# Kernel tuning notes

Measured on AMD Instinct MI355X. Metric: run time of the kernel, lower is better.

## Reference

```python
import jax, jax.numpy as jnp
import numpy as np

N_NODES = 50000
N_EDGES = 800000
IN_CH, HID_CH, OUT_CH = 128, 128, 64


def setup_inputs() -> dict:
    key = jax.random.key(0)
    k1, k2, k3, k4, k5, k6 = jax.random.split(key, 6)
    x = jax.random.normal(k1, (N_NODES, IN_CH), dtype=jnp.float32)
    edge_index = jax.random.randint(k2, (2, N_EDGES), 0, N_NODES, dtype=jnp.int64)
    # nn.Linear params: W [out, in], b [out]
    W1 = jax.random.normal(k3, (HID_CH, IN_CH), dtype=jnp.float32) / np.sqrt(IN_CH)
    b1 = jax.random.normal(k4, (HID_CH,), dtype=jnp.float32) * 0.01
    W2 = jax.random.normal(k5, (OUT_CH, HID_CH), dtype=jnp.float32) / np.sqrt(HID_CH)
    b2 = jax.random.normal(k6, (OUT_CH,), dtype=jnp.float32) * 0.01
    return {"x": x, "edge_index": edge_index, "W1": W1, "b1": b1, "W2": W2, "b2": b2}


def _aggregate(x, edge_index):
    # Faithful to SimpleGNN.aggregate: deg from ROW counts, normalization gathered at DST (col).
    row, col = edge_index[0], edge_index[1]
    n = x.shape[0]
    deg = jnp.bincount(row, length=n).astype(x.dtype)
    deg_inv = jnp.where(deg > 0, 1.0 / deg, 0.0)
    # out[dst] += x[src] * deg_inv[dst]  ==  segment_sum(x[src] by dst) * deg_inv[dst]
    agg = jax.ops.segment_sum(x[row], col, num_segments=n)
    return agg * deg_inv[:, None]


def reference(x, edge_index, W1, b1, W2, b2):
    h = x @ W1.T + b1                 # [N, hidden]
    h = _aggregate(h, edge_index)     # degree-normalized scatter-add
    out = h @ W2.T + b2               # [N, out]
    return out
```

## Files before the change

kernel.cpp:

```cpp
#include <hip/hip_runtime.h>
#include <hip/hip_bf16.h>


#define IN_CH   128
#define OUT_CH  64
#define NCHUNK  128
#define LGCHUNK 7
#define NRANGE  4
#define RBINS   12544
#define MC_BLOCKS 33

typedef unsigned short u16;
typedef unsigned int u32;

static __device__ inline float bfu32_lo(u32 u) {
    u32 v = u << 16; return __uint_as_float(v);
}
static __device__ inline float bfu32_hi(u32 u) {
    u32 v = u & 0xffff0000u; return __uint_as_float(v);
}
static __device__ inline u16 f2bf(float f) {
    __hip_bfloat16 h = __float2bfloat16(f);
    return *reinterpret_cast<u16*>(&h);
}

static __device__ inline int detect_stride(const int* ei) {
    int f = 1;
    for (int i = 1; i < 64; i += 2)
        if (ei[i] != 0) { f = 0; break; }
    return 1 + f;
}

__global__ __launch_bounds__(256) void mk_prep(const float* __restrict__ W1,
                                               const float* __restrict__ b1,
                                               const float* __restrict__ W2,
                                               const int* __restrict__ ei,
                                               float* __restrict__ M,
                                               float* __restrict__ c,
                                               u16* __restrict__ row_slab,
                                               u16* __restrict__ col_slab,
                                               int n_edges, int n_nodes) {
    __shared__ u32 bins[RBINS];
    __shared__ int s_stride;
    int b = blockIdx.x;
    if (b < MC_BLOCKS) {
        int tid = b * 256 + threadIdx.x;
        if (tid < IN_CH * OUT_CH) {
            int o = tid & (OUT_CH - 1);
            int i = tid >> 6;
            float acc = 0.f;
            for (int h = 0; h < 128; ++h)
                acc += W1[h * 128 + i] * W2[o * 128 + h];
            M[i * OUT_CH + o] = acc;
        } else if (tid < IN_CH * OUT_CH + OUT_CH) {
            int o = tid - IN_CH * OUT_CH;
            float acc = 0.f;
            for (int h = 0; h < 128; ++h)
                acc += b1[h] * W2[o * 128 + h];
            c[o] = acc;
        }
        return;
    }
    int hb = b - MC_BLOCKS;
    int chunk = hb & (NCHUNK - 1);
    int range = hb >> LGCHUNK;

    int range_size = (n_nodes + NRANGE - 1) / NRANGE;
    int lo = range * range_size;
    int hi = lo + range_size; if (hi > n_nodes) hi = n_nodes;
    int nbins = hi - lo;
    if (nbins <= 0) return;

    if (threadIdx.x == 0) s_stride = detect_stride(ei);
    for (int i = threadIdx.x; i < nbins; i += 256) bins[i] = 0u;
    __syncthreads();
    int stride = s_stride;

    size_t e0 = (size_t)chunk * n_edges / NCHUNK;
    size_t e1 = (size_t)(chunk + 1) * n_edges / NCHUNK;
    size_t cnt = e1 - e0;
    const int* rp = ei;
    const int* cp = ei + (size_t)n_edges * stride;

    size_t i = threadIdx.x;
    int s[8], d[8];
    for (; i + 1792 < cnt; i += 2048) {
#pragma unroll
        for (int k = 0; k < 8; ++k) s[k] = rp[(e0 + i + 256 * k) * stride];
#pragma unroll
        for (int k = 0; k < 8; ++k) d[k] = cp[(e0 + i + 256 * k) * stride];
#pragma unroll
        for (int k = 0; k < 8; ++k) {
            if (s[k] >= lo && s[k] < hi) atomicAdd(&bins[s[k] - lo], 1u);
            if (d[k] >= lo && d[k] < hi && (unsigned)s[k] < (unsigned)n_nodes)
                atomicAdd(&bins[d[k] - lo], 0x10000u);
        }
    }
    for (; i < cnt; i += 256) {
        int ss = rp[(e0 + i) * stride];
        int dd = cp[(e0 + i) * stride];
        if (ss >= lo && ss < hi) atomicAdd(&bins[ss - lo], 1u);
        if (dd >= lo && dd < hi && (unsigned)ss < (unsigned)n_nodes)
            atomicAdd(&bins[dd - lo], 0x10000u);
    }
    __syncthreads();

    size_t base = (size_t)chunk * n_nodes + lo;
    for (int k = threadIdx.x; k < nbins; k += 256) {
        u32 v = bins[k];
        row_slab[base + k] = (u16)(v & 0xFFFFu);
        col_slab[base + k] = (u16)(v >> 16);
    }
}

__global__ __launch_bounds__(256) void mk_y_choff(const float* __restrict__ x,
                                                  const float* __restrict__ M,
                                                  u16* __restrict__ y,
                                                  u16* __restrict__ row_slab,
                                                  u16* __restrict__ col_slab,
                                                  int* __restrict__ deg_row,
                                                  int* __restrict__ cnt_col,
                                                  int* __restrict__ cursor_part,
                                                  int* __restrict__ bsums,
                                                  int n_nodes, int y_blocks) {
    __shared__ float smem[IN_CH * OUT_CH + 64 * (IN_CH + 4)];
    int b = blockIdx.x;
    int tid = threadIdx.x;

    if (b < y_blocks) {
        float* Ms = smem;
        float (*xs)[IN_CH + 4] = (float(*)[IN_CH + 4])(smem + IN_CH * OUT_CH);
        int tx = tid & 15;
        int ty = tid >> 4;
        int row0 = b * 64;

        const float4* Mv = (const float4*)M;
        float4* Msv = (float4*)Ms;
#pragma unroll
        for (int k = 0; k < 8; ++k) Msv[tid + 256 * k] = Mv[tid + 256 * k];

        for (int f = tid; f < 64 * 32; f += 256) {
            int r = f >> 5, kq = f & 31;
            float4 v = make_float4(0.f, 0.f, 0.f, 0.f);
            if (row0 + r < n_nodes)
                v = *(const float4*)&x[(size_t)(row0 + r) * IN_CH + 4 * kq];
            *(float4*)&xs[r][4 * kq] = v;
        }
        __syncthreads();

        float4 acc[4];
#pragma unroll
        for (int j = 0; j < 4; ++j) acc[j] = make_float4(0.f, 0.f, 0.f, 0.f);

        for (int k = 0; k < IN_CH; k += 4) {
            float4 xr[4], mr[4];
#pragma unroll
            for (int j = 0; j < 4; ++j)
                xr[j] = *(const float4*)&xs[4 * ty + j][k];
#pragma unroll
            for (int kk = 0; kk < 4; ++kk)
                mr[kk] = *(const float4*)&Ms[(k + kk) * OUT_CH + 4 * tx];
#pragma unroll
            for (int j = 0; j < 4; ++j) {
                acc[j].x = fmaf(xr[j].x, mr[0].x, acc[j].x);
                acc[j].y = fmaf(xr[j].x, mr[0].y, acc[j].y);
                acc[j].z = fmaf(xr[j].x, mr[0].z, acc[j].z);
                acc[j].w = fmaf(xr[j].x, mr[0].w, acc[j].w);
                acc[j].x = fmaf(xr[j].y, mr[1].x, acc[j].x);
                acc[j].y = fmaf(xr[j].y, mr[1].y, acc[j].y);
                acc[j].z = fmaf(xr[j].y, mr[1].z, acc[j].z);
                acc[j].w = fmaf(xr[j].y, mr[1].w, acc[j].w);
                acc[j].x = fmaf(xr[j].z, mr[2].x, acc[j].x);
                acc[j].y = fmaf(xr[j].z, mr[2].y, acc[j].y);
                acc[j].z = fmaf(xr[j].z, mr[2].z, acc[j].z);
                acc[j].w = fmaf(xr[j].z, mr[2].w, acc[j].w);
                acc[j].x = fmaf(xr[j].w, mr[3].x, acc[j].x);
                acc[j].y = fmaf(xr[j].w, mr[3].y, acc[j].y);
                acc[j].z = fmaf(xr[j].w, mr[3].z, acc[j].z);
                acc[j].w = fmaf(xr[j].w, mr[3].w, acc[j].w);
            }
        }

#pragma unroll
        for (int j = 0; j < 4; ++j) {
            int r = row0 + 4 * ty + j;
            if (r < n_nodes) {
                ushort4 s4;
                s4.x = f2bf(acc[j].x);
                s4.y = f2bf(acc[j].y);
                s4.z = f2bf(acc[j].z);
                s4.w = f2bf(acc[j].w);
                *(ushort4*)&y[(size_t)r * OUT_CH + 4 * tx] = s4;
            }
        }
        return;
    }

    int* sm = (int*)smem;
    int t = tid;
    int n = (b - y_blocks) * 256 + t;
    int run = 0;
    if (n < n_nodes) {
        int sum = 0;
#pragma unroll 8
        for (int ch = 0; ch < NCHUNK; ++ch)
            sum += row_slab[(size_t)ch * n_nodes + n];
        deg_row[n] = sum;
#pragma unroll 8
        for (int ch = 0; ch < NCHUNK; ++ch) {
            int v = col_slab[(size_t)ch * n_nodes + n];
            col_slab[(size_t)ch * n_nodes + n] = (u16)run;
            run += v;
        }
        cnt_col[n] = run;
    }
    sm[t] = run;
    __syncthreads();
    for (int d = 1; d < 256; d <<= 1) {
        int add = (t >= d) ? sm[t - d] : 0;
        __syncthreads();
        sm[t] += add;
        __syncthreads();
    }
    if (n < n_nodes) cursor_part[n] = sm[t] - run;
    if (t == 255) bsums[b - y_blocks] = sm[t];
}

static __device__ inline void block_bscan(const int* __restrict__ bsums, int nb,
                                          int* __restrict__ bscan) {
    int t = threadIdx.x;
    int v = (t < nb) ? bsums[t] : 0;
    bscan[t] = v;
    __syncthreads();
    for (int d = 1; d < 256; d <<= 1) {
        int add = (t >= d) ? bscan[t - d] : 0;
        __syncthreads();
        bscan[t] += add;
        __syncthreads();
    }
    bscan[t] -= v;
    __syncthreads();
}

__global__ __launch_bounds__(256) void mk_place(const int* __restrict__ ei,
                                                const int* __restrict__ cursor_part,
                                                const int* __restrict__ bsums,
                                                const u16* __restrict__ col_slab,
                                                int* __restrict__ csr_src,
                                                int n_edges, int n_nodes, int nb) {
    __shared__ int rank[RBINS];
    __shared__ int bscan[256];
    block_bscan(bsums, nb, bscan);

    int b = blockIdx.x;
    int chunk = b & (NCHUNK - 1);
    int range = b >> LGCHUNK;

    int range_size = (n_nodes + NRANGE - 1) / NRANGE;
    int lo = range * range_size;
    int hi = lo + range_size; if (hi > n_nodes) hi = n_nodes;
    if (hi <= lo) return;

    for (int i = threadIdx.x; i < hi - lo; i += 256) rank[i] = 0;
    __syncthreads();

    int stride = detect_stride(ei);
    size_t e0 = (size_t)chunk * n_edges / NCHUNK;
    size_t e1 = (size_t)(chunk + 1) * n_edges / NCHUNK;
    size_t cnt = e1 - e0;
    const int* rp = ei;
    const int* cp = ei + (size_t)n_edges * stride;
    size_t slab_base = (size_t)chunk * n_nodes;

    size_t i = threadIdx.x;
    int s[8], d[8], cpart[8], coff[8];
    for (; i + 1792 < cnt; i += 2048) {
#pragma unroll
        for (int k = 0; k < 8; ++k) s[k] = rp[(e0 + i + 256 * k) * stride];
#pragma unroll
        for (int k = 0; k < 8; ++k) d[k] = cp[(e0 + i + 256 * k) * stride];
#pragma unroll
        for (int k = 0; k < 8; ++k) {
            int dc = (d[k] >= lo && d[k] < hi) ? d[k] : lo;
            cpart[k] = cursor_part[dc];
            coff[k]  = (int)col_slab[slab_base + dc];
        }
#pragma unroll
        for (int k = 0; k < 8; ++k) {
            if (d[k] >= lo && d[k] < hi && (unsigned)s[k] < (unsigned)n_nodes) {
                int r = atomicAdd(&rank[d[k] - lo], 1);
                csr_src[cpart[k] + bscan[d[k] >> 8] + coff[k] + r] = s[k];
            }
        }
    }
    for (; i < cnt; i += 256) {
        int ss = rp[(e0 + i) * stride];
        int dd = cp[(e0 + i) * stride];
        if (dd >= lo && dd < hi && (unsigned)ss < (unsigned)n_nodes) {
            int r = atomicAdd(&rank[dd - lo], 1);
            csr_src[cursor_part[dd] + bscan[dd >> 8] + (int)col_slab[slab_base + dd] + r] = ss;
        }
    }
}

__global__ __launch_bounds__(256) void mk_agg_final(const int* __restrict__ cursor_part,
                                                    const int* __restrict__ bsums,
                                                    const int* __restrict__ cnt_col,
                                                    const int* __restrict__ csr_src,
                                                    const int* __restrict__ deg_row,
                                                    const uint2* __restrict__ yv,
                                                    const float* __restrict__ c,
                                                    const float* __restrict__ b2,
                                                    float* __restrict__ out,
                                                    int n_nodes, int nb) {
    __shared__ int bscan[256];
    block_bscan(bsums, nb, bscan);

    int wave = threadIdx.x >> 6;
    int lane = threadIdx.x & 63;
    int dsub = lane >> 4;
    int ch   = lane & 15;
    int d = blockIdx.x * 16 + wave * 4 + dsub;
    if (d >= n_nodes) return;

    int start = cursor_part[d] + bscan[d >> 8];
    int cnt = cnt_col[d];
    int end = start + cnt;
    int e1m = end - 1;
    float a0 = 0.f, a1 = 0.f, a2 = 0.f, a3 = 0.f;
    for (int j = start; j < end; j += 8) {
        int idx[8], srcs[8];
#pragma unroll
        for (int k = 0; k < 8; ++k) {
            int t = j + k;
            idx[k] = t > e1m ? e1m : t;
        }
#pragma unroll
        for (int k = 0; k < 8; ++k) srcs[k] = csr_src[idx[k]];
        uint2 u[8];
#pragma unroll
        for (int k = 0; k < 8; ++k) u[k] = yv[(size_t)srcs[k] * 16 + ch];
#pragma unroll
        for (int k = 1; k < 8; ++k)
            if (j + k >= end) { u[k].x = 0u; u[k].y = 0u; }
#pragma unroll
        for (int k = 0; k < 8; ++k) {
            a0 += bfu32_lo(u[k].x);
            a1 += bfu32_hi(u[k].x);
            a2 += bfu32_lo(u[k].y);
            a3 += bfu32_hi(u[k].y);
        }
    }
    int dr = deg_row[d];
    float di = (dr > 0) ? (1.0f / (float)dr) : 0.f;
    float fc = di * (float)cnt;
    float4 cv = ((const float4*)c)[ch];
    float4 bv = ((const float4*)b2)[ch];
    float4 o;
    o.x = di * a0 + fc * cv.x + bv.x;
    o.y = di * a1 + fc * cv.y + bv.y;
    o.z = di * a2 + fc * cv.z + bv.z;
    o.w = di * a3 + fc * cv.w + bv.w;
    ((float4*)(out + (size_t)d * OUT_CH))[ch] = o;
}

extern "C" void kernel_launch(void* const* d_in, const int* in_sizes, int n_in,
                              void* d_out, int out_size, void* d_ws, size_t ws_size,
                              hipStream_t stream) {
    const float* x  = (const float*)d_in[0];
    const int*   ei = (const int*)d_in[1];
    const float* W1 = (const float*)d_in[2];
    const float* b1 = (const float*)d_in[3];
    const float* W2 = (const float*)d_in[4];
    const float* b2 = (const float*)d_in[5];
    float* out = (float*)d_out;

    const int n_nodes = in_sizes[0] / IN_CH;
    const int n_edges = in_sizes[1] / 2;

    const size_t slab_bytes = (((size_t)NCHUNK * n_nodes * 2) + 127) & ~(size_t)127;
    const size_t csr_bytes  = ((size_t)n_edges * 4 + 127) & ~(size_t)127;

    char* ws = (char*)d_ws;
    float* M        = (float*)(ws);
    float* c        = (float*)(ws + 32768);
    int*   deg_row  = (int*)  (ws + 33152);
    int*   cnt_col  = (int*)  (ws + 233216);
    int*   cursor   = (int*)  (ws + 433280);
    int*   bsums    = (int*)  (ws + 633344);
    u16*   row_slab = (u16*)  (ws + 637440);
    u16*   col_slab = (u16*)  (ws + 637440 + slab_bytes);
    int*   csr_src  = (int*)  (ws + 637440 + 2 * slab_bytes);
    u16*   y        = (u16*)  (ws + 637440 + 2 * slab_bytes + csr_bytes);

    const int y_blocks = (n_nodes + 63) / 64;
    const int nb = (n_nodes + 255) / 256;

    mk_prep<<<MC_BLOCKS + NCHUNK * NRANGE, 256, 0, stream>>>(
        W1, b1, W2, ei, M, c, row_slab, col_slab, n_edges, n_nodes);

    mk_y_choff<<<y_blocks + nb, 256, 0, stream>>>(
        x, M, y, row_slab, col_slab, deg_row, cnt_col, cursor, bsums,
        n_nodes, y_blocks);

    mk_place<<<NCHUNK * NRANGE, 256, 0, stream>>>(
        ei, cursor, bsums, col_slab, csr_src, n_edges, n_nodes, nb);

    mk_agg_final<<<(n_nodes + 15) / 16, 256, 0, stream>>>(
        cursor, bsums, cnt_col, csr_src, deg_row, (const uint2*)y, c, b2, out,
        n_nodes, nb);
}
```

Baseline: 163.7 us.

## Fuse four pipeline kernels into one cooperative persistent kernel with grid syncs

Replaces the four separate launches (prep/histogram, y-GEMM plus count offsets, CSR placement, aggregation) with one cooperative kernel of 512 blocks. The stages are separated by grid-wide barriers, and blocks loop over the work items of each stage. NCHUNK drops from 128 to 112 so the histogram and placement stages fit inside the persistent grid, and stride detection now uses a wave ballot. The aim is to remove kernel launch gaps and tail effects between stages. In exchange, grid syncs cost time, and the persistent grid of 2 blocks per CU with large LDS may limit latency hiding in the gather-heavy aggregation. If the cooperative launch fails, the code falls back to the old four-kernel path.

New measurement: 371.8 us. 2.27x slower.

```diff
diff --git a/kernel.cpp b/kernel.cpp
--- a/kernel.cpp
+++ b/kernel.cpp
@@ -1,80 +1,74 @@
 #include <hip/hip_runtime.h>
 #include <hip/hip_bf16.h>
+#include <hip/hip_cooperative_groups.h>
+
+namespace cg = cooperative_groups;
 
 
 #define IN_CH   128
 #define OUT_CH  64
-#define NCHUNK  128
-#define LGCHUNK 7
+#define NCHUNK  112
 #define NRANGE  4
 #define RBINS   12544
 #define MC_BLOCKS 33
+#define GRID    512
+#define SMEM_FLOATS (IN_CH * OUT_CH + 64 * (IN_CH + 4))
 
 typedef unsigned short u16;
 typedef unsigned int u32;
 
-static __device__ inline float bfu32_lo(u32 u) {
-    u32 v = u << 16; return __uint_as_float(v);
-}
-static __device__ inline float bfu32_hi(u32 u) {
-    u32 v = u & 0xffff0000u; return __uint_as_float(v);
-}
+static __device__ inline float bfu32_lo(u32 u) { return __uint_as_float(u << 16); }
+static __device__ inline float bfu32_hi(u32 u) { return __uint_as_float(u & 0xffff0000u); }
 static __device__ inline u16 f2bf(float f) {
     __hip_bfloat16 h = __float2bfloat16(f);
     return *reinterpret_cast<u16*>(&h);
 }
 
-static __device__ inline int detect_stride(const int* ei) {
-    int f = 1;
-    for (int i = 1; i < 64; i += 2)
-        if (ei[i] != 0) { f = 0; break; }
-    return 1 + f;
-}
-
-__global__ __launch_bounds__(256) void mk_prep(const float* __restrict__ W1,
-                                               const float* __restrict__ b1,
-                                               const float* __restrict__ W2,
-                                               const int* __restrict__ ei,
-                                               float* __restrict__ M,
-                                               float* __restrict__ c,
-                                               u16* __restrict__ row_slab,
-                                               u16* __restrict__ col_slab,
-                                               int n_edges, int n_nodes) {
-    __shared__ u32 bins[RBINS];
-    __shared__ int s_stride;
-    int b = blockIdx.x;
-    if (b < MC_BLOCKS) {
-        int tid = b * 256 + threadIdx.x;
-        if (tid < IN_CH * OUT_CH) {
-            int o = tid & (OUT_CH - 1);
-            int i = tid >> 6;
-            float acc = 0.f;
-            for (int h = 0; h < 128; ++h)
-                acc += W1[h * 128 + i] * W2[o * 128 + h];
-            M[i * OUT_CH + o] = acc;
-        } else if (tid < IN_CH * OUT_CH + OUT_CH) {
-            int o = tid - IN_CH * OUT_CH;
-            float acc = 0.f;
-            for (int h = 0; h < 128; ++h)
-                acc += b1[h] * W2[o * 128 + h];
-            c[o] = acc;
-        }
-        return;
-    }
-    int hb = b - MC_BLOCKS;
-    int chunk = hb & (NCHUNK - 1);
-    int range = hb >> LGCHUNK;
-
+static __device__ inline int detect_stride_wave(const int* __restrict__ ei) {
+    int lane = threadIdx.x & 63;
+    int idx = (lane < 32) ? (2 * lane + 1) : 1;
+    int v = ei[idx];
+    unsigned long long m = __ballot((v != 0) && (lane < 32));
+    return (m == 0ull) ? 2 : 1;
+}
+
+static __device__ void ph_Mc(int b, int tid,
+                             const float* __restrict__ W1, const float* __restrict__ b1,
+                             const float* __restrict__ W2,
+                             float* __restrict__ M, float* __restrict__ c) {
+    int t = b * 256 + tid;
+    if (t < IN_CH * OUT_CH) {
+        int o = t & (OUT_CH - 1);
+        int i = t >> 6;
+        float acc = 0.f;
+        for (int h = 0; h < 128; ++h)
+            acc += W1[h * 128 + i] * W2[o * 128 + h];
+        M[i * OUT_CH + o] = acc;
+    } else if (t < IN_CH * OUT_CH + OUT_CH) {
+        int o = t - IN_CH * OUT_CH;
+        float acc = 0.f;
+        for (int h = 0; h < 128; ++h)
+            acc += b1[h] * W2[o * 128 + h];
+        c[o] = acc;
+    }
+}
+
+static __device__ void ph_hist(int j, int tid, float* __restrict__ smem,
+                               const int* __restrict__ ei,
+                               u16* __restrict__ row_slab, u16* __restrict__ col_slab,
+                               int n_edges, int n_nodes) {
+    u32* bins = (u32*)smem;
+    int chunk = j % NCHUNK;
+    int range = j / NCHUNK;
     int range_size = (n_nodes + NRANGE - 1) / NRANGE;
     int lo = range * range_size;
     int hi = lo + range_size; if (hi > n_nodes) hi = n_nodes;
     int nbins = hi - lo;
     if (nbins <= 0) return;
 
-    if (threadIdx.x == 0) s_stride = detect_stride(ei);
-    for (int i = threadIdx.x; i < nbins; i += 256) bins[i] = 0u;
-    __syncthreads();
-    int stride = s_stride;
+    int stride = detect_stride_wave(ei);
+    for (int i = tid; i < nbins; i += 256) bins[i] = 0u;
+    __syncthreads();
 
     size_t e0 = (size_t)chunk * n_edges / NCHUNK;
     size_t e1 = (size_t)(chunk + 1) * n_edges / NCHUNK;
@@ -82,7 +76,7 @@
     const int* rp = ei;
     const int* cp = ei + (size_t)n_edges * stride;
 
-    size_t i = threadIdx.x;
+    size_t i = tid;
     int s[8], d[8];
     for (; i + 1792 < cnt; i += 2048) {
 #pragma unroll
@@ -106,99 +100,92 @@
     __syncthreads();
 
     size_t base = (size_t)chunk * n_nodes + lo;
-    for (int k = threadIdx.x; k < nbins; k += 256) {
+    for (int k = tid; k < nbins; k += 256) {
         u32 v = bins[k];
         row_slab[base + k] = (u16)(v & 0xFFFFu);
         col_slab[base + k] = (u16)(v >> 16);
     }
 }
 
-__global__ __launch_bounds__(256) void mk_y_choff(const float* __restrict__ x,
-                                                  const float* __restrict__ M,
-                                                  u16* __restrict__ y,
-                                                  u16* __restrict__ row_slab,
-                                                  u16* __restrict__ col_slab,
-                                                  int* __restrict__ deg_row,
-                                                  int* __restrict__ cnt_col,
-                                                  int* __restrict__ cursor_part,
-                                                  int* __restrict__ bsums,
-                                                  int n_nodes, int y_blocks) {
-    __shared__ float smem[IN_CH * OUT_CH + 64 * (IN_CH + 4)];
-    int b = blockIdx.x;
-    int tid = threadIdx.x;
-
-    if (b < y_blocks) {
-        float* Ms = smem;
-        float (*xs)[IN_CH + 4] = (float(*)[IN_CH + 4])(smem + IN_CH * OUT_CH);
-        int tx = tid & 15;
-        int ty = tid >> 4;
-        int row0 = b * 64;
-
-        const float4* Mv = (const float4*)M;
-        float4* Msv = (float4*)Ms;
-#pragma unroll
-        for (int k = 0; k < 8; ++k) Msv[tid + 256 * k] = Mv[tid + 256 * k];
-
-        for (int f = tid; f < 64 * 32; f += 256) {
-            int r = f >> 5, kq = f & 31;
-            float4 v = make_float4(0.f, 0.f, 0.f, 0.f);
-            if (row0 + r < n_nodes)
-                v = *(const float4*)&x[(size_t)(row0 + r) * IN_CH + 4 * kq];
-            *(float4*)&xs[r][4 * kq] = v;
-        }
-        __syncthreads();
-
-        float4 acc[4];
-#pragma unroll
-        for (int j = 0; j < 4; ++j) acc[j] = make_float4(0.f, 0.f, 0.f, 0.f);
-
-        for (int k = 0; k < IN_CH; k += 4) {
-            float4 xr[4], mr[4];
-#pragma unroll
-            for (int j = 0; j < 4; ++j)
-                xr[j] = *(const float4*)&xs[4 * ty + j][k];
-#pragma unroll
-            for (int kk = 0; kk < 4; ++kk)
-                mr[kk] = *(const float4*)&Ms[(k + kk) * OUT_CH + 4 * tx];
-#pragma unroll
-            for (int j = 0; j < 4; ++j) {
-                acc[j].x = fmaf(xr[j].x, mr[0].x, acc[j].x);
-                acc[j].y = fmaf(xr[j].x, mr[0].y, acc[j].y);
-                acc[j].z = fmaf(xr[j].x, mr[0].z, acc[j].z);
-                acc[j].w = fmaf(xr[j].x, mr[0].w, acc[j].w);
-                acc[j].x = fmaf(xr[j].y, mr[1].x, acc[j].x);
-                acc[j].y = fmaf(xr[j].y, mr[1].y, acc[j].y);
-                acc[j].z = fmaf(xr[j].y, mr[1].z, acc[j].z);
-                acc[j].w = fmaf(xr[j].y, mr[1].w, acc[j].w);
-                acc[j].x = fmaf(xr[j].z, mr[2].x, acc[j].x);
-                acc[j].y = fmaf(xr[j].z, mr[2].y, acc[j].y);
-                acc[j].z = fmaf(xr[j].z, mr[2].z, acc[j].z);
-                acc[j].w = fmaf(xr[j].z, mr[2].w, acc[j].w);
-                acc[j].x = fmaf(xr[j].w, mr[3].x, acc[j].x);
-                acc[j].y = fmaf(xr[j].w, mr[3].y, acc[j].y);
-                acc[j].z = fmaf(xr[j].w, mr[3].z, acc[j].z);
-                acc[j].w = fmaf(xr[j].w, mr[3].w, acc[j].w);
-            }
-        }
-
+static __device__ void ph_ytile(int t, int tid, float* __restrict__ smem,
+                                const float* __restrict__ x, const float* __restrict__ M,
+                                u16* __restrict__ y, int n_nodes) {
+    __syncthreads();
+    float* Ms = smem;
+    float (*xs)[IN_CH + 4] = (float(*)[IN_CH + 4])(smem + IN_CH * OUT_CH);
+    int tx = tid & 15;
+    int ty = tid >> 4;
+    int row0 = t * 64;
+
+    const float4* Mv = (const float4*)M;
+    float4* Msv = (float4*)Ms;
+#pragma unroll
+    for (int k = 0; k < 8; ++k) Msv[tid + 256 * k] = Mv[tid + 256 * k];
+
+    for (int f = tid; f < 64 * 32; f += 256) {
+        int r = f >> 5, kq = f & 31;
+        float4 v = make_float4(0.f, 0.f, 0.f, 0.f);
+        if (row0 + r < n_nodes)
+            v = *(const float4*)&x[(size_t)(row0 + r) * IN_CH + 4 * kq];
+        *(float4*)&xs[r][4 * kq] = v;
+    }
+    __syncthreads();
+
+    float4 acc[4];
+#pragma unroll
+    for (int j = 0; j < 4; ++j) acc[j] = make_float4(0.f, 0.f, 0.f, 0.f);
+
+    for (int k = 0; k < IN_CH; k += 4) {
+        float4 xr[4], mr[4];
+#pragma unroll
+        for (int j = 0; j < 4; ++j)
+            xr[j] = *(const float4*)&xs[4 * ty + j][k];
+#pragma unroll
+        for (int kk = 0; kk < 4; ++kk)
+            mr[kk] = *(const float4*)&Ms[(k + kk) * OUT_CH + 4 * tx];
 #pragma unroll
         for (int j = 0; j < 4; ++j) {
-            int r = row0 + 4 * ty + j;
-            if (r < n_nodes) {
-                ushort4 s4;
-                s4.x = f2bf(acc[j].x);
-                s4.y = f2bf(acc[j].y);
-                s4.z = f2bf(acc[j].z);
-                s4.w = f2bf(acc[j].w);
-                *(ushort4*)&y[(size_t)r * OUT_CH + 4 * tx] = s4;
-            }
-        }
-        return;
-    }
-
+            acc[j].x = fmaf(xr[j].x, mr[0].x, acc[j].x);
+            acc[j].y = fmaf(xr[j].x, mr[0].y, acc[j].y);
+            acc[j].z = fmaf(xr[j].x, mr[0].z, acc[j].z);
+            acc[j].w = fmaf(xr[j].x, mr[0].w, acc[j].w);
+            acc[j].x = fmaf(xr[j].y, mr[1].x, acc[j].x);
+            acc[j].y = fmaf(xr[j].y, mr[1].y, acc[j].y);
+            acc[j].z = fmaf(xr[j].y, mr[1].z, acc[j].z);
+            acc[j].w = fmaf(xr[j].y, mr[1].w, acc[j].w);
+            acc[j].x = fmaf(xr[j].z, mr[2].x, acc[j].x);
+            acc[j].y = fmaf(xr[j].z, mr[2].y, acc[j].y);
+            acc[j].z = fmaf(xr[j].z, mr[2].z, acc[j].z);
+            acc[j].w = fmaf(xr[j].z, mr[2].w, acc[j].w);
+            acc[j].x = fmaf(xr[j].w, mr[3].x, acc[j].x);
+            acc[j].y = fmaf(xr[j].w, mr[3].y, acc[j].y);
+            acc[j].z = fmaf(xr[j].w, mr[3].z, acc[j].z);
+            acc[j].w = fmaf(xr[j].w, mr[3].w, acc[j].w);
+        }
+    }
+
+#pragma unroll
+    for (int j = 0; j < 4; ++j) {
+        int r = row0 + 4 * ty + j;
+        if (r < n_nodes) {
+            ushort4 s4;
+            s4.x = f2bf(acc[j].x);
+            s4.y = f2bf(acc[j].y);
+            s4.z = f2bf(acc[j].z);
+            s4.w = f2bf(acc[j].w);
+            *(ushort4*)&y[(size_t)r * OUT_CH + 4 * tx] = s4;
+        }
+    }
+}
+
+static __device__ void ph_choff(int jj, int tid, float* __restrict__ smem,
+                                u16* __restrict__ row_slab, u16* __restrict__ col_slab,
+                                int* __restrict__ deg_row, int* __restrict__ cnt_col,
+                                int* __restrict__ cursor_part, int* __restrict__ bsums,
+                                int n_nodes) {
+    __syncthreads();
     int* sm = (int*)smem;
-    int t = tid;
-    int n = (b - y_blocks) * 256 + t;
+    int n = jj * 256 + tid;
     int run = 0;
     if (n < n_nodes) {
         int sum = 0;
@@ -214,20 +201,20 @@
         }
         cnt_col[n] = run;
     }
-    sm[t] = run;
+    sm[tid] = run;
     __syncthreads();
     for (int d = 1; d < 256; d <<= 1) {
-        int add = (t >= d) ? sm[t - d] : 0;
+        int add = (tid >= d) ? sm[tid - d] : 0;
         __syncthreads();
-        sm[t] += add;
+        sm[tid] += add;
         __syncthreads();
     }
-    if (n < n_nodes) cursor_part[n] = sm[t] - run;
-    if (t == 255) bsums[b - y_blocks] = sm[t];
-}
-
-static __device__ inline void block_bscan(const int* __restrict__ bsums, int nb,
-                                          int* __restrict__ bscan) {
+    if (n < n_nodes) cursor_part[n] = sm[tid] - run;
+    if (tid == 255) bsums[jj] = sm[tid];
+}
+
+static __device__ void block_bscan(const int* __restrict__ bsums, int nb,
+                                   int* __restrict__ bscan) {
     int t = threadIdx.x;
     int v = (t < nb) ? bsums[t] : 0;
     bscan[t] = v;
@@ -242,29 +229,28 @@
     __syncthreads();
 }
 
-__global__ __launch_bounds__(256) void mk_place(const int* __restrict__ ei,
-                                                const int* __restrict__ cursor_part,
-                                                const int* __restrict__ bsums,
-                                                const u16* __restrict__ col_slab,
-                                                int* __restrict__ csr_src,
-                                                int n_edges, int n_nodes, int nb) {
-    __shared__ int rank[RBINS];
-    __shared__ int bscan[256];
+static __device__ void ph_place(int j, int tid, float* __restrict__ smem,
+                                const int* __restrict__ ei,
+                                const int* __restrict__ cursor_part,
+                                const int* __restrict__ bsums,
+                                const u16* __restrict__ col_slab,
+                                int* __restrict__ csr_src,
+                                int n_edges, int n_nodes, int nb) {
+    int* rank = (int*)smem;
+    int* bscan = (int*)smem + RBINS;
     block_bscan(bsums, nb, bscan);
 
-    int b = blockIdx.x;
-    int chunk = b & (NCHUNK - 1);
-    int range = b >> LGCHUNK;
-
+    int chunk = j % NCHUNK;
+    int range = j / NCHUNK;
     int range_size = (n_nodes + NRANGE - 1) / NRANGE;
     int lo = range * range_size;
     int hi = lo + range_size; if (hi > n_nodes) hi = n_nodes;
     if (hi <= lo) return;
 
-    for (int i = threadIdx.x; i < hi - lo; i += 256) rank[i] = 0;
-    __syncthreads();
-
-    int stride = detect_stride(ei);
+    int stride = detect_stride_wave(ei);
+    for (int i = tid; i < hi - lo; i += 256) rank[i] = 0;
+    __syncthreads();
+
     size_t e0 = (size_t)chunk * n_edges / NCHUNK;
     size_t e1 = (size_t)(chunk + 1) * n_edges / NCHUNK;
     size_t cnt = e1 - e0;
@@ -272,7 +258,7 @@
     const int* cp = ei + (size_t)n_edges * stride;
     size_t slab_base = (size_t)chunk * n_nodes;
 
-    size_t i = threadIdx.x;
+    size_t i = tid;
     int s[8], d[8], cpart[8], coff[8];
     for (; i + 1792 < cnt; i += 2048) {
 #pragma unroll
@@ -303,24 +289,17 @@
     }
 }
 
-__global__ __launch_bounds__(256) void mk_agg_final(const int* __restrict__ cursor_part,
-                                                    const int* __restrict__ bsums,
-                                                    const int* __restrict__ cnt_col,
-                                                    const int* __restrict__ csr_src,
-                                                    const int* __restrict__ deg_row,
-                                                    const uint2* __restrict__ yv,
-                                                    const float* __restrict__ c,
-                                                    const float* __restrict__ b2,
-                                                    float* __restrict__ out,
-                                                    int n_nodes, int nb) {
-    __shared__ int bscan[256];
-    block_bscan(bsums, nb, bscan);
-
-    int wave = threadIdx.x >> 6;
-    int lane = threadIdx.x & 63;
-    int dsub = lane >> 4;
-    int ch   = lane & 15;
-    int d = blockIdx.x * 16 + wave * 4 + dsub;
+static __device__ void ph_agg(int g, int tid, const int* __restrict__ bscan,
+                              const int* __restrict__ cursor_part,
+                              const int* __restrict__ cnt_col,
+                              const int* __restrict__ csr_src,
+                              const int* __restrict__ deg_row,
+                              const uint2* __restrict__ yv,
+                              const float* __restrict__ c, const float* __restrict__ b2,
+                              float* __restrict__ out, int n_nodes) {
+    int sub = tid >> 4;
+    int ch  = tid & 15;
+    int d = g * 16 + sub;
     if (d >= n_nodes) return;
 
     int start = cursor_part[d] + bscan[d >> 8];
@@ -364,6 +343,115 @@
     ((float4*)(out + (size_t)d * OUT_CH))[ch] = o;
 }
 
+__global__ __launch_bounds__(256) void gnn_fused(const float* __restrict__ x,
+                                                 const int* __restrict__ ei,
+                                                 const float* __restrict__ W1,
+                                                 const float* __restrict__ b1,
+                                                 const float* __restrict__ W2,
+                                                 const float* __restrict__ b2,
+                                                 float* __restrict__ out,
+                                                 float* __restrict__ M,
+                                                 float* __restrict__ c,
+                                                 int* __restrict__ deg_row,
+                                                 int* __restrict__ cnt_col,
+                                                 int* __restrict__ cursor_part,
+                                                 int* __restrict__ bsums,
+                                                 u16* __restrict__ row_slab,
+                                                 u16* __restrict__ col_slab,
+                                                 int* __restrict__ csr_src,
+                                                 u16* __restrict__ y,
+                                                 int n_nodes, int n_edges) {
+    __shared__ float smem[SMEM_FLOATS];
+    cg::grid_group grid = cg::this_grid();
+    int b = blockIdx.x, tid = threadIdx.x;
+    int y_blocks = (n_nodes + 63) >> 6;
+    int nb = (n_nodes + 255) >> 8;
+
+    if (b < MC_BLOCKS) ph_Mc(b, tid, W1, b1, W2, M, c);
+    else if (b < MC_BLOCKS + NCHUNK * NRANGE)
+        ph_hist(b - MC_BLOCKS, tid, smem, ei, row_slab, col_slab, n_edges, n_nodes);
+    grid.sync();
+
+    int njobs = y_blocks + nb;
+    for (int j = b; j < njobs; j += gridDim.x) {
+        if (j < y_blocks) ph_ytile(j, tid, smem, x, M, y, n_nodes);
+        else ph_choff(j - y_blocks, tid, smem, row_slab, col_slab, deg_row,
+                      cnt_col, cursor_part, bsums, n_nodes);
+    }
+    grid.sync();
+
+    if (b < NCHUNK * NRANGE)
+        ph_place(b, tid, smem, ei, cursor_part, bsums, col_slab, csr_src,
+                 n_edges, n_nodes, nb);
+    grid.sync();
+
+    int* bscan = (int*)smem;
+    block_bscan(bsums, nb, bscan);
+    int ngroups = (n_nodes + 15) >> 4;
+    for (int g = b; g < ngroups; g += gridDim.x)
+        ph_agg(g, tid, bscan, cursor_part, cnt_col, csr_src, deg_row,
+               (const uint2*)y, c, b2, out, n_nodes);
+}
+
+__global__ __launch_bounds__(256) void k_prep(const float* __restrict__ W1,
+                                              const float* __restrict__ b1,
+                                              const float* __restrict__ W2,
+                                              const int* __restrict__ ei,
+                                              float* __restrict__ M, float* __restrict__ c,
+                                              u16* __restrict__ row_slab,
+                                              u16* __restrict__ col_slab,
+                                              int n_edges, int n_nodes) {
+    __shared__ float smem[SMEM_FLOATS];
+    int b = blockIdx.x;
+    if (b < MC_BLOCKS) ph_Mc(b, threadIdx.x, W1, b1, W2, M, c);
+    else ph_hist(b - MC_BLOCKS, threadIdx.x, smem, ei, row_slab, col_slab,
+                 n_edges, n_nodes);
+}
+
+__global__ __launch_bounds__(256) void k_ych(const float* __restrict__ x,
+                                             const float* __restrict__ M,
+                                             u16* __restrict__ y,
+                                             u16* __restrict__ row_slab,
+                                             u16* __restrict__ col_slab,
+                                             int* __restrict__ deg_row,
+                                             int* __restrict__ cnt_col,
+                                             int* __restrict__ cursor_part,
+                                             int* __restrict__ bsums,
+                                             int n_nodes, int y_blocks) {
+    __shared__ float smem[SMEM_FLOATS];
+    int j = blockIdx.x;
+    if (j < y_blocks) ph_ytile(j, threadIdx.x, smem, x, M, y, n_nodes);
+    else ph_choff(j - y_blocks, threadIdx.x, smem, row_slab, col_slab, deg_row,
+                  cnt_col, cursor_part, bsums, n_nodes);
+}
+
+__global__ __launch_bounds__(256) void k_place(const int* __restrict__ ei,
+                                               const int* __restrict__ cursor_part,
+                                               const int* __restrict__ bsums,
+                                               const u16* __restrict__ col_slab,
+                                               int* __restrict__ csr_src,
+                                               int n_edges, int n_nodes, int nb) {
+    __shared__ float smem[SMEM_FLOATS];
+    ph_place(blockIdx.x, threadIdx.x, smem, ei, cursor_part, bsums, col_slab,
+             csr_src, n_edges, n_nodes, nb);
+}
+
+__global__ __launch_bounds__(256) void k_agg(const int* __restrict__ cursor_part,
+                                             const int* __restrict__ bsums,
+                                             const int* __restrict__ cnt_col,
+                                             const int* __restrict__ csr_src,
+                                             const int* __restrict__ deg_row,
+                                             const uint2* __restrict__ yv,
+                                             const float* __restrict__ c,
+                                             const float* __restrict__ b2,
+                                             float* __restrict__ out,
+                                             int n_nodes, int nb) {
+    __shared__ int bscan[256];
+    block_bscan(bsums, nb, bscan);
+    ph_agg(blockIdx.x, threadIdx.x, bscan, cursor_part, cnt_col, csr_src,
+           deg_row, yv, c, b2, out, n_nodes);
+}
+
 extern "C" void kernel_launch(void* const* d_in, const int* in_sizes, int n_in,
                               void* d_out, int out_size, void* d_ws, size_t ws_size,
                               hipStream_t stream) {
@@ -375,8 +463,8 @@
     const float* b2 = (const float*)d_in[5];
     float* out = (float*)d_out;
 
-    const int n_nodes = in_sizes[0] / IN_CH;
-    const int n_edges = in_sizes[1] / 2;
+    int n_nodes = in_sizes[0] / IN_CH;
+    int n_edges = in_sizes[1] / 2;
 
     const size_t slab_bytes = (((size_t)NCHUNK * n_nodes * 2) + 127) & ~(size_t)127;
     const size_t csr_bytes  = ((size_t)n_edges * 4 + 127) & ~(size_t)127;
@@ -393,20 +481,27 @@
     int*   csr_src  = (int*)  (ws + 637440 + 2 * slab_bytes);
     u16*   y        = (u16*)  (ws + 637440 + 2 * slab_bytes + csr_bytes);
 
-    const int y_blocks = (n_nodes + 63) / 64;
-    const int nb = (n_nodes + 255) / 256;
-
-    mk_prep<<<MC_BLOCKS + NCHUNK * NRANGE, 256, 0, stream>>>(
-        W1, b1, W2, ei, M, c, row_slab, col_slab, n_edges, n_nodes);
-
-    mk_y_choff<<<y_blocks + nb, 256, 0, stream>>>(
-        x, M, y, row_slab, col_slab, deg_row, cnt_col, cursor, bsums,
-        n_nodes, y_blocks);
-
-    mk_place<<<NCHUNK * NRANGE, 256, 0, stream>>>(
-        ei, cursor, bsums, col_slab, csr_src, n_edges, n_nodes, nb);
-
-    mk_agg_final<<<(n_nodes + 15) / 16, 256, 0, stream>>>(
-        cursor, bsums, cnt_col, csr_src, deg_row, (const uint2*)y, c, b2, out,
-        n_nodes, nb);
-}
+    int y_blocks = (n_nodes + 63) / 64;
+    int nb = (n_nodes + 255) / 256;
+
+    void* args[] = {
+        (void*)&x, (void*)&ei, (void*)&W1, (void*)&b1, (void*)&W2, (void*)&b2,
+        (void*)&out, (void*)&M, (void*)&c, (void*)&deg_row, (void*)&cnt_col,
+        (void*)&cursor, (void*)&bsums, (void*)&row_slab, (void*)&col_slab,
+        (void*)&csr_src, (void*)&y, (void*)&n_nodes, (void*)&n_edges
+    };
+    hipError_t err = hipLaunchCooperativeKernel((void*)gnn_fused, dim3(GRID),
+                                                dim3(256), args, 0, stream);
+    if (err != hipSuccess) {
+        k_prep<<<MC_BLOCKS + NCHUNK * NRANGE, 256, 0, stream>>>(
+            W1, b1, W2, ei, M, c, row_slab, col_slab, n_edges, n_nodes);
+        k_ych<<<y_blocks + nb, 256, 0, stream>>>(
+            x, M, y, row_slab, col_slab, deg_row, cnt_col, cursor, bsums,
+            n_nodes, y_blocks);
+        k_place<<<NCHUNK * NRANGE, 256, 0, stream>>>(
+            ei, cursor, bsums, col_slab, csr_src, n_edges, n_nodes, nb);
+        k_agg<<<(n_nodes + 15) / 16, 256, 0, stream>>>(
+            cursor, bsums, cnt_col, csr_src, deg_row, (const uint2*)y, c, b2,
+            out, n_nodes, nb);
+    }
+}
```

## Split node ranges finer, halve GEMM rows per block, ballot-based stride detect

Applied to the files above, without the earlier changes.

Doubles the node-range partitioning (NRANGE 4→8) so each histogram/placement block uses half the LDS bins, which allows more resident blocks per CU but makes each block rescan its edge chunk for twice as many ranges. The y GEMM tile drops from 64 to 32 rows per block, giving more blocks and fewer accumulators per thread at the cost of reloading M into LDS more often. Stride detection becomes a wave ballot instead of a serial single-thread loop, which also removes one shared variable and an extra serialization point.

Measured after the change: 165.9 us. About the same (+1.3%).

```diff
diff --git a/kernel.cpp b/kernel.cpp
--- a/kernel.cpp
+++ b/kernel.cpp
@@ -6,29 +6,27 @@
 #define OUT_CH  64
 #define NCHUNK  128
 #define LGCHUNK 7
-#define NRANGE  4
-#define RBINS   12544
+#define NRANGE  8
+#define RBINS   6272
 #define MC_BLOCKS 33
+#define YROWS   32
 
 typedef unsigned short u16;
 typedef unsigned int u32;
 
-static __device__ inline float bfu32_lo(u32 u) {
-    u32 v = u << 16; return __uint_as_float(v);
-}
-static __device__ inline float bfu32_hi(u32 u) {
-    u32 v = u & 0xffff0000u; return __uint_as_float(v);
-}
+static __device__ inline float bfu32_lo(u32 u) { return __uint_as_float(u << 16); }
+static __device__ inline float bfu32_hi(u32 u) { return __uint_as_float(u & 0xffff0000u); }
 static __device__ inline u16 f2bf(float f) {
     __hip_bfloat16 h = __float2bfloat16(f);
     return *reinterpret_cast<u16*>(&h);
 }
 
-static __device__ inline int detect_stride(const int* ei) {
-    int f = 1;
-    for (int i = 1; i < 64; i += 2)
-        if (ei[i] != 0) { f = 0; break; }
-    return 1 + f;
+static __device__ inline int detect_stride_wave(const int* __restrict__ ei) {
+    int lane = threadIdx.x & 63;
+    int idx = (lane < 32) ? (2 * lane + 1) : 1;
+    int v = ei[idx];
+    unsigned long long m = __ballot((v != 0) && (lane < 32));
+    return (m == 0ull) ? 2 : 1;
 }
 
 __global__ __launch_bounds__(256) void mk_prep(const float* __restrict__ W1,
@@ -41,19 +39,19 @@
                                                u16* __restrict__ col_slab,
                                                int n_edges, int n_nodes) {
     __shared__ u32 bins[RBINS];
-    __shared__ int s_stride;
     int b = blockIdx.x;
+    int tid = threadIdx.x;
     if (b < MC_BLOCKS) {
-        int tid = b * 256 + threadIdx.x;
-        if (tid < IN_CH * OUT_CH) {
-            int o = tid & (OUT_CH - 1);
-            int i = tid >> 6;
+        int t = b * 256 + tid;
+        if (t < IN_CH * OUT_CH) {
+            int o = t & (OUT_CH - 1);
+            int i = t >> 6;
             float acc = 0.f;
             for (int h = 0; h < 128; ++h)
                 acc += W1[h * 128 + i] * W2[o * 128 + h];
             M[i * OUT_CH + o] = acc;
-        } else if (tid < IN_CH * OUT_CH + OUT_CH) {
-            int o = tid - IN_CH * OUT_CH;
+        } else if (t < IN_CH * OUT_CH + OUT_CH) {
+            int o = t - IN_CH * OUT_CH;
             float acc = 0.f;
             for (int h = 0; h < 128; ++h)
                 acc += b1[h] * W2[o * 128 + h];
@@ -71,10 +69,9 @@
     int nbins = hi - lo;
     if (nbins <= 0) return;
 
-    if (threadIdx.x == 0) s_stride = detect_stride(ei);
-    for (int i = threadIdx.x; i < nbins; i += 256) bins[i] = 0u;
-    __syncthreads();
-    int stride = s_stride;
+    int stride = detect_stride_wave(ei);
+    for (int i = tid; i < nbins; i += 256) bins[i] = 0u;
+    __syncthreads();
 
     size_t e0 = (size_t)chunk * n_edges / NCHUNK;
     size_t e1 = (size_t)(chunk + 1) * n_edges / NCHUNK;
@@ -82,7 +79,7 @@
     const int* rp = ei;
     const int* cp = ei + (size_t)n_edges * stride;
 
-    size_t i = threadIdx.x;
+    size_t i = tid;
     int s[8], d[8];
     for (; i + 1792 < cnt; i += 2048) {
 #pragma unroll
@@ -106,7 +103,7 @@
     __syncthreads();
 
     size_t base = (size_t)chunk * n_nodes + lo;
-    for (int k = threadIdx.x; k < nbins; k += 256) {
+    for (int k = tid; k < nbins; k += 256) {
         u32 v = bins[k];
         row_slab[base + k] = (u16)(v & 0xFFFFu);
         col_slab[base + k] = (u16)(v >> 16);
@@ -123,7 +120,7 @@
                                                   int* __restrict__ cursor_part,
                                                   int* __restrict__ bsums,
                                                   int n_nodes, int y_blocks) {
-    __shared__ float smem[IN_CH * OUT_CH + 64 * (IN_CH + 4)];
+    __shared__ float smem[IN_CH * OUT_CH + YROWS * (IN_CH + 4)];
     int b = blockIdx.x;
     int tid = threadIdx.x;
 
@@ -132,14 +129,14 @@
         float (*xs)[IN_CH + 4] = (float(*)[IN_CH + 4])(smem + IN_CH * OUT_CH);
         int tx = tid & 15;
         int ty = tid >> 4;
-        int row0 = b * 64;
+        int row0 = b * YROWS;
 
         const float4* Mv = (const float4*)M;
         float4* Msv = (float4*)Ms;
 #pragma unroll
         for (int k = 0; k < 8; ++k) Msv[tid + 256 * k] = Mv[tid + 256 * k];
 
-        for (int f = tid; f < 64 * 32; f += 256) {
+        for (int f = tid; f < YROWS * 32; f += 256) {
             int r = f >> 5, kq = f & 31;
             float4 v = make_float4(0.f, 0.f, 0.f, 0.f);
             if (row0 + r < n_nodes)
@@ -148,50 +145,47 @@
         }
         __syncthreads();
 
-        float4 acc[4];
-#pragma unroll
-        for (int j = 0; j < 4; ++j) acc[j] = make_float4(0.f, 0.f, 0.f, 0.f);
+        float4 acc0 = make_float4(0.f, 0.f, 0.f, 0.f);
+        float4 acc1 = make_float4(0.f, 0.f, 0.f, 0.f);
 
         for (int k = 0; k < IN_CH; k += 4) {
-            float4 xr[4], mr[4];
-#pragma unroll
-            for (int j = 0; j < 4; ++j)
-                xr[j] = *(const float4*)&xs[4 * ty + j][k];
-#pragma unroll
-            for (int kk = 0; kk < 4; ++kk)
-                mr[kk] = *(const float4*)&Ms[(k + kk) * OUT_CH + 4 * tx];
-#pragma unroll
-            for (int j = 0; j < 4; ++j) {
-                acc[j].x = fmaf(xr[j].x, mr[0].x, acc[j].x);
-                acc[j].y = fmaf(xr[j].x, mr[0].y, acc[j].y);
-                acc[j].z = fmaf(xr[j].x, mr[0].z, acc[j].z);
-                acc[j].w = fmaf(xr[j].x, mr[0].w, acc[j].w);
-                acc[j].x = fmaf(xr[j].y, mr[1].x, acc[j].x);
-                acc[j].y = fmaf(xr[j].y, mr[1].y, acc[j].y);
-                acc[j].z = fmaf(xr[j].y, mr[1].z, acc[j].z);
-                acc[j].w = fmaf(xr[j].y, mr[1].w, acc[j].w);
-                acc[j].x = fmaf(xr[j].z, mr[2].x, acc[j].x);
-                acc[j].y = fmaf(xr[j].z, mr[2].y, acc[j].y);
-                acc[j].z = fmaf(xr[j].z, mr[2].z, acc[j].z);
-                acc[j].w = fmaf(xr[j].z, mr[2].w, acc[j].w);
-                acc[j].x = fmaf(xr[j].w, mr[3].x, acc[j].x);
-                acc[j].y = fmaf(xr[j].w, mr[3].y, acc[j].y);
-                acc[j].z = fmaf(xr[j].w, mr[3].z, acc[j].z);
-                acc[j].w = fmaf(xr[j].w, mr[3].w, acc[j].w);
-            }
-        }
-
-#pragma unroll
-        for (int j = 0; j < 4; ++j) {
-            int r = row0 + 4 * ty + j;
-            if (r < n_nodes) {
-                ushort4 s4;
-                s4.x = f2bf(acc[j].x);
-                s4.y = f2bf(acc[j].y);
-                s4.z = f2bf(acc[j].z);
-                s4.w = f2bf(acc[j].w);
-                *(ushort4*)&y[(size_t)r * OUT_CH + 4 * tx] = s4;
-            }
+            float4 xr0 = *(const float4*)&xs[ty][k];
+            float4 xr1 = *(const float4*)&xs[ty + 16][k];
+            float4 m0 = *(const float4*)&Ms[(k + 0) * OUT_CH + 4 * tx];
+            float4 m1 = *(const float4*)&Ms[(k + 1) * OUT_CH + 4 * tx];
+            float4 m2 = *(const float4*)&Ms[(k + 2) * OUT_CH + 4 * tx];
+            float4 m3 = *(const float4*)&Ms[(k + 3) * OUT_CH + 4 * tx];
+            acc0.x = fmaf(xr0.x, m0.x, acc0.x); acc0.y = fmaf(xr0.x, m0.y, acc0.y);
+            acc0.z = fmaf(xr0.x, m0.z, acc0.z); acc0.w = fmaf(xr0.x, m0.w, acc0.w);
+            acc0.x = fmaf(xr0.y, m1.x, acc0.x); acc0.y = fmaf(xr0.y, m1.y, acc0.y);
+            acc0.z = fmaf(xr0.y, m1.z, acc0.z); acc0.w = fmaf(xr0.y, m1.w, acc0.w);
+            acc0.x = fmaf(xr0.z, m2.x, acc0.x); acc0.y = fmaf(xr0.z, m2.y, acc0.y);
+            acc0.z = fmaf(xr0.z, m2.z, acc0.z); acc0.w = fmaf(xr0.z, m2.w, acc0.w);
+            acc0.x = fmaf(xr0.w, m3.x, acc0.x); acc0.y = fmaf(xr0.w, m3.y, acc0.y);
+            acc0.z = fmaf(xr0.w, m3.z, acc0.z); acc0.w = fmaf(xr0.w, m3.w, acc0.w);
+            acc1.x = fmaf(xr1.x, m0.x, acc1.x); acc1.y = fmaf(xr1.x, m0.y, acc1.y);
+            acc1.z = fmaf(xr1.x, m0.z, acc1.z); acc1.w = fmaf(xr1.x, m0.w, acc1.w);
+            acc1.x = fmaf(xr1.y, m1.x, acc1.x); acc1.y = fmaf(xr1.y, m1.y, acc1.y);
+            acc1.z = fmaf(xr1.y, m1.z, acc1.z); acc1.w = fmaf(xr1.y, m1.w, acc1.w);
+            acc1.x = fmaf(xr1.z, m2.x, acc1.x); acc1.y = fmaf(xr1.z, m2.y, acc1.y);
+            acc1.z = fmaf(xr1.z, m2.z, acc1.z); acc1.w = fmaf(xr1.z, m2.w, acc1.w);
+            acc1.x = fmaf(xr1.w, m3.x, acc1.x); acc1.y = fmaf(xr1.w, m3.y, acc1.y);
+            acc1.z = fmaf(xr1.w, m3.z, acc1.z); acc1.w = fmaf(xr1.w, m3.w, acc1.w);
+        }
+
+        int r0 = row0 + ty;
+        int r1 = row0 + ty + 16;
+        if (r0 < n_nodes) {
+            ushort4 s4;
+            s4.x = f2bf(acc0.x); s4.y = f2bf(acc0.y);
+            s4.z = f2bf(acc0.z); s4.w = f2bf(acc0.w);
+            *(ushort4*)&y[(size_t)r0 * OUT_CH + 4 * tx] = s4;
+        }
+        if (r1 < n_nodes) {
+            ushort4 s4;
+            s4.x = f2bf(acc1.x); s4.y = f2bf(acc1.y);
+            s4.z = f2bf(acc1.z); s4.w = f2bf(acc1.w);
+            *(ushort4*)&y[(size_t)r1 * OUT_CH + 4 * tx] = s4;
         }
         return;
     }
@@ -226,8 +220,8 @@
     if (t == 255) bsums[b - y_blocks] = sm[t];
 }
 
-static __device__ inline void block_bscan(const int* __restrict__ bsums, int nb,
-                                          int* __restrict__ bscan) {
+static __device__ void block_bscan(const int* __restrict__ bsums, int nb,
+                                   int* __restrict__ bscan) {
     int t = threadIdx.x;
     int v = (t < nb) ? bsums[t] : 0;
     bscan[t] = v;
@@ -261,10 +255,10 @@
     int hi = lo + range_size; if (hi > n_nodes) hi = n_nodes;
     if (hi <= lo) return;
 
+    int stride = detect_stride_wave(ei);
     for (int i = threadIdx.x; i < hi - lo; i += 256) rank[i] = 0;
     __syncthreads();
 
-    int stride = detect_stride(ei);
     size_t e0 = (size_t)chunk * n_edges / NCHUNK;
     size_t e1 = (size_t)(chunk + 1) * n_edges / NCHUNK;
     size_t cnt = e1 - e0;
@@ -393,7 +387,7 @@
     int*   csr_src  = (int*)  (ws + 637440 + 2 * slab_bytes);
     u16*   y        = (u16*)  (ws + 637440 + 2 * slab_bytes + csr_bytes);
 
-    const int y_blocks = (n_nodes + 63) / 64;
+    const int y_blocks = (n_nodes + YROWS - 1) / YROWS;
     const int nb = (n_nodes + 255) / 256;
 
     mk_prep<<<MC_BLOCKS + NCHUNK * NRANGE, 256, 0, stream>>>(
```
